# Kernel tuning notes

Measured on AMD Instinct MI355X. Metric: run time of the kernel, lower is better.

Reference implementation:

```python
import jax, jax.numpy as jnp
import numpy as np

EPS = 1e-8
LN_EPS = 1e-5
NEG = -1e9
H, E, D, P = 4, 32, 8, 64          # heads, embed_dim, head_dim, particles (= input_dim)
N_LAYERS, N_CLS = 4, 2
N_BATCH = 2048
F_EXTRA = 60                        # x feature channels; F_EXTRA + 4 == P == input_dim


def _ln(x):
    m = jnp.mean(x, -1, keepdims=True)
    v = jnp.mean((x - m) ** 2, -1, keepdims=True)
    return (x - m) * jax.lax.rsqrt(v + LN_EPS)


def _lin(x, w, b):
    return x @ w.T + b


def _gelu(x):
    return jax.nn.gelu(x, approximate=False)


def _mha(q_in, kv, in_w, in_b, out_w, out_b, attn_bias, kpm):
    # torch nn.MultiheadAttention, batch_first=False. q_in: (L,N,E), kv: (S,N,E)
    L, N, _ = q_in.shape
    S = kv.shape[0]
    q = _lin(q_in, in_w[:E], in_b[:E]) * (D ** -0.5)
    k = _lin(kv, in_w[E:2 * E], in_b[E:2 * E])
    v = _lin(kv, in_w[2 * E:], in_b[2 * E:])
    q = q.reshape(L, N, H, D); k = k.reshape(S, N, H, D); v = v.reshape(S, N, H, D)
    s = jnp.einsum('lnhd,snhd->nhls', q, k)
    if attn_bias is not None:
        s = s + attn_bias.reshape(N, H, L, S)
    s = jnp.where(kpm[:, None, None, :], NEG, s)
    a = jax.nn.softmax(s, -1)
    o = jnp.einsum('nhls,snhd->lnhd', a, v).reshape(L, N, E)
    return _lin(o, out_w, out_b)


def _jet_features(v):
    # vectorized calculate_jet_features_; v: (N,4,P). All pair features are symmetric,
    # diagonal stays zero (python loop skipped i==j), features are detached.
    e, px, py, pz = v[:, 0], v[:, 1], v[:, 2], v[:, 3]
    pt = jnp.sqrt(px ** 2 + py ** 2 + EPS)
    y = 0.5 * jnp.log((e + pz + EPS) / (e - pz + EPS))
    phi = jnp.mod(jnp.arctan2(py, px + EPS), 2.0 * np.pi)   # already in [0, 2pi)
    r = lambda a: a[:, :, None]
    c = lambda a: a[:, None, :]
    dist = (r(px) + c(px)) ** 2 + (r(py) + c(py)) ** 2 + (r(pz) + c(pz)) ** 2
    delta = jnp.sqrt(jnp.abs((r(y) - c(y)) ** 2 + (r(phi) - c(phi)) ** 2))
    pmin = jnp.minimum(r(pt), c(pt))
    kt = pmin * delta
    z = pmin / (r(pt) + c(pt) + EPS)
    m2 = r(e) ** 2 + c(e) ** 2 - dist
    f = jnp.stack([delta, kt, z, m2], axis=1)               # (N,4,P,P)
    f = f * (1.0 - jnp.eye(v.shape[2], dtype=f.dtype))
    return jax.lax.stop_gradient(f)


def _conv2d(x, w, b, stride, pad):
    y = jax.lax.conv_general_dilated(x, w, (stride, stride), [(pad, pad), (pad, pad)],
                                     dimension_numbers=('NCHW', 'OIHW', 'NCHW'))
    return y + b[None, :, None, None]


def _forward(x, four_momenta, jet_inputs, bn_w, bn_b, e1_w, e1_b, e2_w, e2_b,
             c1_w, c1_b, c2_w, c2_b,
             pb_in_w, pb_in_b, pb_out_w, pb_out_b, pb_f1_w, pb_f1_b, pb_f2_w, pb_f2_b, pb_wres,
             cb_in_w, cb_in_b, cb_out_w, cb_out_b, cb_f1_w, cb_f1_b, cb_f2_w, cb_f2_b, cb_wres,
             cb_cattn, cls_token, norm_w, norm_b, m1_w, m1_b, mh_w, mh_b, mf_w, mf_b):
    N = x.shape[0]
    xc = jnp.concatenate([x, four_momenta], axis=1)                 # (N, P, P): channels == particles
    kpm = ~(jnp.arange(P)[None, :] < jet_inputs[:, 1][:, None])     # (N, P) True = padded key
    xb = jnp.transpose(xc, (0, 2, 1))                               # (N, C=P, L=input_dim)
    mu = jnp.mean(xb, axis=(0, 2), keepdims=True)
    var = jnp.var(xb, axis=(0, 2), keepdims=True)
    xb = (xb - mu) * jax.lax.rsqrt(var + LN_EPS) * bn_w[None, :, None] + bn_b[None, :, None]
    h = jnp.transpose(xb, (2, 0, 1))                                # (seq, N, P)
    h = _gelu(_lin(_ln(h), e1_w, e1_b))
    h = _gelu(_lin(_ln(h), e2_w, e2_b))                             # (P, N, E)
    # --- PairEmbed: pairwise kinematic features -> 2 convs -> per-head attention bias
    f = _jet_features(four_momenta)                                 # (N, 4, P, P)
    cpe = _conv2d(f, c1_w, c1_b, 4, 0)                              # (N, H, 16, 16)
    cpe = _conv2d(cpe, c2_w, c2_b, 2, 1)                            # (N, H, 9, 9)
    bias = cpe.reshape(N * H, 9, 9)
    bias = jnp.pad(bias, ((0, 0), (0, P - 9), (0, P - 9)))          # additive bias zero-padded to (N*H,P,P)
    # --- particle blocks
    for i in range(N_LAYERS):
        res = h
        a = _ln(h)
        a = _mha(a, a, pb_in_w[i], pb_in_b[i], pb_out_w[i], pb_out_b[i], bias, kpm)
        h = _ln(a) + res
        res = h
        g = _gelu(_lin(_ln(h), pb_f1_w[i], pb_f1_b[i]))
        g = _lin(_ln(g), pb_f2_w[i], pb_f2_b[i])
        h = g + pb_wres[i] * res
    # --- class-attention blocks
    kpm_cls = jnp.concatenate([jnp.zeros((N, 1), dtype=bool), kpm], axis=1)
    cls = jnp.broadcast_to(cls_token, (1, N, E))
    for i in range(N_CLS):
        res = cls
        u = _ln(jnp.concatenate([cls, h], axis=0))                  # pre_attn_norm on keys/values only
        a = _mha(cls, u, cb_in_w[i], cb_in_b[i], cb_out_w[i], cb_out_b[i], None, kpm_cls)
        # tbhd,h->tbdh then reshape flattens as (d, h) order, matching torch
        a = jnp.einsum('tbhd,h->tbdh', a.reshape(1, N, H, D), cb_cattn[i]).reshape(1, N, E)
        cls = _ln(a) + res
        res = cls
        g = _gelu(_lin(_ln(cls), cb_f1_w[i], cb_f1_b[i]))
        g = _lin(_ln(g), cb_f2_w[i], cb_f2_b[i])
        cls = g + cb_wres[i] * res
    # --- head: affine LayerNorm + MLP (the two transposes in MLP cancel)
    z = (_ln(cls) * norm_w + norm_b)[0]                             # (N, E)
    z = jax.nn.relu(_lin(z, m1_w, m1_b))
    z = jax.nn.relu(_lin(z, mh_w, mh_b))
    z = jax.nn.sigmoid(_lin(z, mf_w, mf_b))                         # (N, 1)
    return z.reshape(-1)


def setup_inputs():
    key = jax.random.key(0)
    ks = jax.random.split(key, 40)
    w = lambda k, s: (0.05 * jax.random.normal(k, s)).astype(jnp.float32)
    p3 = jax.random.normal(ks[0], (N_BATCH, 3, P), dtype=jnp.float32)
    en = jnp.sqrt(jnp.sum(p3 ** 2, axis=1, keepdims=True) + 0.1)    # physical: E > |pz|
    four_momenta = jnp.concatenate([en, p3], axis=1)
    return {
        'x': jax.random.normal(ks[1], (N_BATCH, F_EXTRA, P), dtype=jnp.float32),
        'four_momenta': four_momenta,
        'jet_inputs': jax.random.randint(ks[2], (N_BATCH, 2), 1, P + 1),
        'bn_w': jnp.ones((P,), jnp.float32), 'bn_b': jnp.zeros((P,), jnp.float32),
        'e1_w': w(ks[3], (64, P)), 'e1_b': w(ks[4], (64,)),
        'e2_w': w(ks[5], (E, 64)), 'e2_b': w(ks[6], (E,)),
        'c1_w': w(ks[7], (H, 4, 4, 4)), 'c1_b': w(ks[8], (H,)),
        'c2_w': w(ks[9], (H, H, 2, 2)), 'c2_b': w(ks[10], (H,)),
        'pb_in_w': w(ks[11], (N_LAYERS, 3 * E, E)), 'pb_in_b': w(ks[12], (N_LAYERS, 3 * E)),
        'pb_out_w': w(ks[13], (N_LAYERS, E, E)), 'pb_out_b': w(ks[14], (N_LAYERS, E)),
        'pb_f1_w': w(ks[15], (N_LAYERS, 2 * E, E)), 'pb_f1_b': w(ks[16], (N_LAYERS, 2 * E)),
        'pb_f2_w': w(ks[17], (N_LAYERS, E, 2 * E)), 'pb_f2_b': w(ks[18], (N_LAYERS, E)),
        'pb_wres': jnp.ones((N_LAYERS, E), jnp.float32),
        'cb_in_w': w(ks[19], (N_CLS, 3 * E, E)), 'cb_in_b': w(ks[20], (N_CLS, 3 * E)),
        'cb_out_w': w(ks[21], (N_CLS, E, E)), 'cb_out_b': w(ks[22], (N_CLS, E)),
        'cb_f1_w': w(ks[23], (N_CLS, 2 * E, E)), 'cb_f1_b': w(ks[24], (N_CLS, 2 * E)),
        'cb_f2_w': w(ks[25], (N_CLS, E, 2 * E)), 'cb_f2_b': w(ks[26], (N_CLS, E)),
        'cb_wres': jnp.ones((N_CLS, E), jnp.float32),
        'cb_cattn': jnp.ones((N_CLS, H), jnp.float32),
        'cls_token': w(ks[27], (1, 1, E)),
        'norm_w': jnp.ones((E,), jnp.float32), 'norm_b': jnp.zeros((E,), jnp.float32),
        'm1_w': w(ks[28], (32, E)), 'm1_b': w(ks[29], (32,)),
        'mh_w': w(ks[30], (32, 32)), 'mh_b': w(ks[31], (32,)),
        'mf_w': w(ks[32], (1, 32)), 'mf_b': w(ks[33], (1,)),
    }


def reference(x, four_momenta, jet_inputs, bn_w, bn_b, e1_w, e1_b, e2_w, e2_b,
              c1_w, c1_b, c2_w, c2_b,
              pb_in_w, pb_in_b, pb_out_w, pb_out_b, pb_f1_w, pb_f1_b, pb_f2_w, pb_f2_b, pb_wres,
              cb_in_w, cb_in_b, cb_out_w, cb_out_b, cb_f1_w, cb_f1_b, cb_f2_w, cb_f2_b, cb_wres,
              cb_cattn, cls_token, norm_w, norm_b, m1_w, m1_b, mh_w, mh_b, mf_w, mf_b):
    return _forward(x, four_momenta, jet_inputs, bn_w, bn_b, e1_w, e1_b, e2_w, e2_b,
                    c1_w, c1_b, c2_w, c2_b,
                    pb_in_w, pb_in_b, pb_out_w, pb_out_b, pb_f1_w, pb_f1_b, pb_f2_w, pb_f2_b, pb_wres,
                    cb_in_w, cb_in_b, cb_out_w, cb_out_b, cb_f1_w, cb_f1_b, cb_f2_w, cb_f2_b, cb_wres,
                    cb_cattn, cls_token, norm_w, norm_b, m1_w, m1_b, mh_w, mh_b, mf_w, mf_b)
```

## Files before the change

### kernel.cpp

```cpp
#include <hip/hip_runtime.h>


__device__ __forceinline__ float4 ld4(const float* p){ return *reinterpret_cast<const float4*>(p); }
__device__ __forceinline__ void st4(float* p, float4 v){ *reinterpret_cast<float4*>(p) = v; }
__device__ __forceinline__ float dot4(float4 a, float4 b){ return a.x*b.x + a.y*b.y + a.z*b.z + a.w*b.w; }
__device__ __forceinline__ float geluf(float v){ return 0.5f*v*(1.0f + erff(v*0.70710678118654752f)); }

__global__ void bn_stats_partial(const float* __restrict__ x, const float* __restrict__ fm,
                                 float* __restrict__ part) {
  int p  = threadIdx.x & 63;
  int rg = threadIdx.x >> 6;
  float s = 0.f, s2 = 0.f;
  for (int R = blockIdx.x*4 + rg; R < 2048*64; R += 1024) {
    int n_ = R >> 6, c = R & 63;
    float v = (c < 60) ? x[n_*3840 + c*64 + p] : fm[n_*256 + (c-60)*64 + p];
    s += v; s2 += v*v;
  }
  __shared__ float sm[256], sm2[256];
  sm[threadIdx.x] = s; sm2[threadIdx.x] = s2;
  __syncthreads();
  if (threadIdx.x < 64) {
    part[blockIdx.x*128 + p]      = sm[p]+sm[64+p]+sm[128+p]+sm[192+p];
    part[blockIdx.x*128 + 64 + p] = sm2[p]+sm2[64+p]+sm2[128+p]+sm2[192+p];
  }
// ... 148 lines not shown
        }
      }
    }
    G_bias[n*324 + idx] = s;
  }
  {
    int p4 = (tid & 15) * 4;
    float sc0 = SSTAT[p4], sc1 = SSTAT[p4+1], sc2 = SSTAT[p4+2], sc3 = SSTAT[p4+3];
    float sh0 = SSTAT[64+p4], sh1 = SSTAT[64+p4+1], sh2 = SSTAT[64+p4+2], sh3 = SSTAT[64+p4+3];
    for (int c = tid>>4; c < 64; c += 16) {
      float4 v = (c < 60) ? ld4(x + n*3840 + c*64 + p4) : ld4(fm + n*256 + (c-60)*64 + p4);
      st4(&SX[c*68 + p4], make_float4(v.x*sc0+sh0, v.y*sc1+sh1, v.z*sc2+sh2, v.w*sc3+sh3));
    }
  }
  __syncthreads();

  if (wact) ln_rows64(SX, SY, tid);
  for (int idx = tid; idx < 1024; idx += 256) st4(&SW[(idx>>4)*68 + (idx&15)*4], ld4(e1w + idx*4));
  if (tid < 64) SW[4352+tid] = e1b[tid];
  __syncthreads();

  {
    int tg = tid>>4, og = tid&15;
    float acc[4][4];
    #pragma unroll
    for (int o=0;o<4;o++){ float b = SW[4352+o*16+og];
      #pragma unroll
      for (int i=0;i<4;i++) acc[i][o] = b; }
    if (wact) {
      #pragma unroll 2
      for (int j=0;j<64;j+=4){
        float4 av[4], wv[4];
        #pragma unroll
        for (int i=0;i<4;i++) av[i] = ld4(SY + (tg*4+i)*68 + j);
        #pragma unroll
        for (int o=0;o<4;o++) wv[o] = ld4(SW + (o*16+og)*68 + j);
        #pragma unroll
        for (int i=0;i<4;i++)
          #pragma unroll
          for (int o=0;o<4;o++) acc[i][o] += dot4(av[i], wv[o]);
      }
    }
    __syncthreads();
    if (wact) {
      #pragma unroll
      for (int i=0;i<4;i++)
        #pragma unroll
        for (int o=0;o<4;o++) SX[(tg*4+i)*68 + o*16+og] = geluf(acc[i][o]);
    }
  }
  __syncthreads();

  if (wact) ln_rows64(SX, SY, tid);
  for (int idx = tid; idx < 512; idx += 256) st4(&SW[(idx>>4)*68 + (idx&15)*4], ld4(e2w + idx*4));
  if (tid < 32) SW[4352+tid] = e2b[tid];
  __syncthreads();

  if (wact) {
    int tg = tid>>4, og = tid&15;
    float acc[4][2];
    #pragma unroll
    for (int o=0;o<2;o++){ float b = SW[4352+o*16+og];
      #pragma unroll
      for (int i=0;i<4;i++) acc[i][o] = b; }
    #pragma unroll 2
    for (int j=0;j<64;j+=4){
      float4 av[4], wv[2];
      #pragma unroll
      for (int i=0;i<4;i++) av[i] = ld4(SY + (tg*4+i)*68 + j);
      #pragma unroll
      for (int o=0;o<2;o++) wv[o] = ld4(SW + (o*16+og)*68 + j);
      #pragma unroll
      for (int i=0;i<4;i++)
        #pragma unroll
        for (int o=0;o<2;o++) acc[i][o] += dot4(av[i], wv[o]);
    }
    #pragma unroll
    for (int i=0;i<4;i++)
      #pragma unroll
      for (int o=0;o<2;o++) G_h[n*2048 + (tg*4+i)*32 + o*16+og] = geluf(acc[i][o]);
  }
}

__global__ __launch_bounds__(256, 4) void k_layer(
    const int* __restrict__ ji,
    const float* __restrict__ in_w,  const float* __restrict__ in_b,
    const float* __restrict__ out_w, const float* __restrict__ out_b,
    const float* __restrict__ f1w,   const float* __restrict__ f1b,
    const float* __restrict__ f2w,   const float* __restrict__ f2b,
    const float* __restrict__ wres,
    float* __restrict__ G_h, const float* __restrict__ G_bias)
{
  const int n   = blockIdx.x;
  const int tid = threadIdx.x;
  const int njet = ji[n*2+1];
  const bool wact = ((tid>>6)<<4) < njet;
  const int r_ = tid>>2, g_ = tid&3;

  __shared__ __align__(16) float SX[64*36];
  __shared__ __align__(16) float SY[64*68];
  __shared__ __align__(16) float SW[3584];

  float b9[9];
  {
    int hh = tid>>6, l = tid&63;
    if (l < 9) {
      #pragma unroll
      for (int j=0;j<9;j++) b9[j] = G_bias[n*324 + hh*81 + l*9 + j];
    } else {
      #pragma unroll
      for (int j=0;j<9;j++) b9[j] = 0.f;
    }
  }
  float4 h0 = make_float4(0,0,0,0), h1 = make_float4(0,0,0,0);
  if (wact) {
    h0 = ld4(G_h + n*2048 + r_*32 + g_*8);
    h1 = ld4(G_h + n*2048 + r_*32 + g_*8 + 4);
  }

  if (wact) {
    float s = h0.x+h0.y+h0.z+h0.w + h1.x+h1.y+h1.z+h1.w;
    s += __shfl_xor(s,1); s += __shfl_xor(s,2);
    float mean = s * 0.03125f;
    float4 da = make_float4(h0.x-mean,h0.y-mean,h0.z-mean,h0.w-mean);
    float4 db = make_float4(h1.x-mean,h1.y-mean,h1.z-mean,h1.w-mean);
    float q = dot4(da,da) + dot4(db,db);
    q += __shfl_xor(q,1); q += __shfl_xor(q,2);
    float irs = rsqrtf(q*0.03125f + 1e-5f);
    st4(&SX[r_*36 + g_*8],   make_float4(da.x*irs, da.y*irs, da.z*irs, da.w*irs));
    st4(&SX[r_*36 + g_*8+4], make_float4(db.x*irs, db.y*irs, db.z*irs, db.w*irs));
  }
  for (int idx = tid; idx < 768; idx += 256) st4(&SW[(idx>>3)*36 + (idx&7)*4], ld4(in_w + idx*4));
  if (tid < 96) SW[3456+tid] = in_b[tid];
  __syncthreads();

  if (wact) {
    int tg = tid>>4, og = tid&15;
    float acc[4][4];
    #pragma unroll
    for (int o=0;o<4;o++){ float b = SW[3456+32+o*16+og];
      #pragma unroll
      for (int i=0;i<4;i++) acc[i][o] = b; }
    #pragma unroll 2
    for (int j=0;j<32;j+=4){
      float4 av[4], wv[4];
      #pragma unroll
      for (int i=0;i<4;i++) av[i] = ld4(SX + (tg*4+i)*36 + j);
      #pragma unroll
      for (int o=0;o<4;o++) wv[o] = ld4(SW + (32+o*16+og)*36 + j);
      #pragma unroll
      for (int i=0;i<4;i++)
        #pragma unroll
        for (int o=0;o<4;o++) acc[i][o] += dot4(av[i], wv[o]);
    }
    #pragma unroll
    for (int i=0;i<4;i++)
      #pragma unroll
      for (int o=0;o<4;o++){
        int ew = 32 + o*16+og, t = tg*4+i;
        if (ew < 64) SY[(ew-32)*68 + t] = acc[i][o];
        else         SY[2176 + (ew-64)*68 + t] = acc[i][o];
      }
  }
  __syncthreads();

  float od[8];
  {
    int hh = tid>>6, l = tid&63;
    float qd[8];
    #pragma unroll
    for (int d=0;d<8;d++){
      int e = hh*8+d;
      float a_ = SW[3456+e];
      #pragma unroll
      for (int k=0;k<8;k++) a_ += dot4(ld4(SX + l*36 + k*4), ld4(SW + e*36 + k*4));
      qd[d] = a_ * 0.35355339059327373f;
    }
    float m = -3.4e38f, lsum = 0.f;
    #pragma unroll
    for (int d=0;d<8;d++) od[d] = 0.f;
    #pragma unroll 1
    for (int s0 = 0; s0 < njet; s0 += 16) {
      float sc[16];
      #pragma unroll
      for (int j=0;j<16;j++) sc[j]=0.f;
      #pragma unroll
      for (int d=0;d<8;d++){
        const float* kr = SY + (hh*8+d)*68 + s0;
        float qv = qd[d];
        #pragma unroll
        for (int j=0;j<16;j+=4){
          float4 kv4 = ld4(kr+j);
          sc[j]  +=qv*kv4.x; sc[j+1]+=qv*kv4.y;
          sc[j+2]+=qv*kv4.z; sc[j+3]+=qv*kv4.w;
        }
      }
      float cm = -3.4e38f;
      if (s0 != 0 && s0 + 16 <= njet) {
        #pragma unroll
        for (int j=0;j<16;j++) cm = fmaxf(cm, sc[j]);
      } else {
        #pragma unroll
        for (int j=0;j<16;j++){
          int s = s0+j;
          float a_ = sc[j];
          if (s0 == 0 && l < 9 && j < 9) a_ += b9[j];
          a_ = (s >= njet) ? -1000000000.0f : a_;
          sc[j] = a_;
          cm = fmaxf(cm, a_);
        }
      }
      float nm = fmaxf(m, cm);
      float corr = __expf(m - nm);
      lsum *= corr;
      #pragma unroll
      for (int d=0;d<8;d++) od[d] *= corr;
      #pragma unroll
      for (int j=0;j<16;j++){ sc[j] = __expf(sc[j]-nm); lsum += sc[j]; }
      #pragma unroll
      for (int d=0;d<8;d++){
        const float* vr = SY + 2176 + (hh*8+d)*68 + s0;
        float a_ = 0.f;
        #pragma unroll
        for (int j=0;j<16;j+=4){
          float4 vv = ld4(vr+j);
          a_ += sc[j]*vv.x + sc[j+1]*vv.y + sc[j+2]*vv.z + sc[j+3]*vv.w;
        }
        od[d] += a_;
      }
      m = nm;
    }
    float inv = 1.f/lsum;
    #pragma unroll
    for (int d=0;d<8;d++) od[d] *= inv;
  }
  __syncthreads();
  {
    int hh = tid>>6, l = tid&63;
    st4(&SX[l*36 + hh*8],     make_float4(od[0],od[1],od[2],od[3]));
    st4(&SX[l*36 + hh*8 + 4], make_float4(od[4],od[5],od[6],od[7]));
  }
  for (int idx = tid; idx < 256; idx += 256) st4(&SW[(idx>>3)*36 + (idx&7)*4], ld4(out_w + idx*4));
  if (tid < 32) SW[3456+tid] = out_b[tid];
  __syncthreads();

  if (wact) {
    int tg = tid>>4, og = tid&15;
    float acc[4][2];
    #pragma unroll
    for (int o=0;o<2;o++){ float b = SW[3456+o*16+og];
      #pragma unroll
      for (int i=0;i<4;i++) acc[i][o] = b; }
    #pragma unroll 2
    for (int j=0;j<32;j+=4){
      float4 av[4], wv[2];
      #pragma unroll
      for (int i=0;i<4;i++) av[i] = ld4(SX + (tg*4+i)*36 + j);
      #pragma unroll
      for (int o=0;o<2;o++) wv[o] = ld4(SW + (o*16+og)*36 + j);
      #pragma unroll
      for (int i=0;i<4;i++)
        #pragma unroll
        for (int o=0;o<2;o++) acc[i][o] += dot4(av[i], wv[o]);
    }
    #pragma unroll
    for (int i=0;i<4;i++)
      #pragma unroll
      for (int o=0;o<2;o++) SY[(tg*4+i)*36 + o*16+og] = acc[i][o];
  }
  __syncthreads();

  if (wact) {
    const float* row = SY + r_*36 + g_*8;
    float4 a = ld4(row), b = ld4(row+4);
    float s = a.x+a.y+a.z+a.w + b.x+b.y+b.z+b.w;
    s += __shfl_xor(s,1); s += __shfl_xor(s,2);
    float mean = s * 0.03125f;
    float4 da = make_float4(a.x-mean,a.y-mean,a.z-mean,a.w-mean);
    float4 db = make_float4(b.x-mean,b.y-mean,b.z-mean,b.w-mean);
    float q = dot4(da,da) + dot4(db,db);
    q += __shfl_xor(q,1); q += __shfl_xor(q,2);
    float irs = rsqrtf(q*0.03125f + 1e-5f);
    h0 = make_float4(da.x*irs+h0.x, da.y*irs+h0.y, da.z*irs+h0.z, da.w*irs+h0.w);
    h1 = make_float4(db.x*irs+h1.x, db.y*irs+h1.y, db.z*irs+h1.z, db.w*irs+h1.w);
    float s2 = h0.x+h0.y+h0.z+h0.w + h1.x+h1.y+h1.z+h1.w;
    s2 += __shfl_xor(s2,1); s2 += __shfl_xor(s2,2);
    float mean2 = s2 * 0.03125f;
    float4 ea = make_float4(h0.x-mean2,h0.y-mean2,h0.z-mean2,h0.w-mean2);
    float4 eb = make_float4(h1.x-mean2,h1.y-mean2,h1.z-mean2,h1.w-mean2);
    float q2 = dot4(ea,ea) + dot4(eb,eb);
    q2 += __shfl_xor(q2,1); q2 += __shfl_xor(q2,2);
    float irs2 = rsqrtf(q2*0.03125f + 1e-5f);
    st4(&SX[r_*36 + g_*8],   make_float4(ea.x*irs2, ea.y*irs2, ea.z*irs2, ea.w*irs2));
    st4(&SX[r_*36 + g_*8+4], make_float4(eb.x*irs2, eb.y*irs2, eb.z*irs2, eb.w*irs2));
  }
  for (int idx = tid; idx < 512; idx += 256) st4(&SW[(idx>>3)*36 + (idx&7)*4], ld4(f1w + idx*4));
  if (tid < 64) SW[3456+tid] = f1b[tid];
  __syncthreads();

  if (wact) {
    int tg = tid>>4, og = tid&15;
    float acc[4][4];
    #pragma unroll
    for (int o=0;o<4;o++){ float b = SW[3456+o*16+og];
      #pragma unroll
      for (int i=0;i<4;i++) acc[i][o] = b; }
    #pragma unroll 2
    for (int j=0;j<32;j+=4){
      float4 av[4], wv[4];
      #pragma unroll
      for (int i=0;i<4;i++) av[i] = ld4(SX + (tg*4+i)*36 + j);
      #pragma unroll
      for (int o=0;o<4;o++) wv[o] = ld4(SW + (o*16+og)*36 + j);
      #pragma unroll
      for (int i=0;i<4;i++)
        #pragma unroll
        for (int o=0;o<4;o++) acc[i][o] += dot4(av[i], wv[o]);
    }
    #pragma unroll
    for (int i=0;i<4;i++)
      #pragma unroll
      for (int o=0;o<4;o++) SY[(tg*4+i)*68 + o*16+og] = geluf(acc[i][o]);
  }
  __syncthreads();

  if (wact) {
    float* row = SY + r_*68 + g_*16;
    float4 v0 = ld4(row), v1 = ld4(row+4), v2 = ld4(row+8), v3 = ld4(row+12);
    float s = v0.x+v0.y+v0.z+v0.w + v1.x+v1.y+v1.z+v1.w
            + v2.x+v2.y+v2.z+v2.w + v3.x+v3.y+v3.z+v3.w;
    s += __shfl_xor(s,1); s += __shfl_xor(s,2);
    float mean = s * 0.015625f;
    float4 d0 = make_float4(v0.x-mean,v0.y-mean,v0.z-mean,v0.w-mean);
    float4 d1 = make_float4(v1.x-mean,v1.y-mean,v1.z-mean,v1.w-mean);
    float4 d2 = make_float4(v2.x-mean,v2.y-mean,v2.z-mean,v2.w-mean);
    float4 d3 = make_float4(v3.x-mean,v3.y-mean,v3.z-mean,v3.w-mean);
    float q = dot4(d0,d0)+dot4(d1,d1)+dot4(d2,d2)+dot4(d3,d3);
    q += __shfl_xor(q,1); q += __shfl_xor(q,2);
    float irs = rsqrtf(q*0.015625f + 1e-5f);
    st4(row,    make_float4(d0.x*irs,d0.y*irs,d0.z*irs,d0.w*irs));
    st4(row+4,  make_float4(d1.x*irs,d1.y*irs,d1.z*irs,d1.w*irs));
    st4(row+8,  make_float4(d2.x*irs,d2.y*irs,d2.z*irs,d2.w*irs));
    st4(row+12, make_float4(d3.x*irs,d3.y*irs,d3.z*irs,d3.w*irs));
  }
  for (int idx = tid; idx < 512; idx += 256) st4(&SW[(idx>>4)*68 + (idx&15)*4], ld4(f2w + idx*4));
  if (tid < 32){ SW[3456+tid] = f2b[tid]; SW[3488+tid] = wres[tid]; }
  __syncthreads();

  if (wact) {
    int tg = tid>>4, og = tid&15;
    float acc[4][2];
    #pragma unroll
    for (int o=0;o<2;o++){ float b = SW[3456+o*16+og];
      #pragma unroll
      for (int i=0;i<4;i++) acc[i][o] = b; }
    #pragma unroll 2
    for (int j=0;j<64;j+=4){
      float4 av[4], wv[2];
      #pragma unroll
      for (int i=0;i<4;i++) av[i] = ld4(SY + (tg*4+i)*68 + j);
      #pragma unroll
      for (int o=0;o<2;o++) wv[o] = ld4(SW + (o*16+og)*68 + j);
      #pragma unroll
      for (int i=0;i<4;i++)
        #pragma unroll
        for (int o=0;o<2;o++) acc[i][o] += dot4(av[i], wv[o]);
    }
    #pragma unroll
    for (int i=0;i<4;i++)
      #pragma unroll
      for (int o=0;o<2;o++) SX[(tg*4+i)*36 + o*16+og] = acc[i][o];
  }
  __syncthreads();

  if (wact) {
    float4 a0 = ld4(&SX[r_*36 + g_*8]),  a1 = ld4(&SX[r_*36 + g_*8 + 4]);
    float4 w0 = ld4(&SW[3488 + g_*8]),   w1 = ld4(&SW[3488 + g_*8 + 4]);
    st4(G_h + n*2048 + r_*32 + g_*8,
        make_float4(a0.x + w0.x*h0.x, a0.y + w0.y*h0.y, a0.z + w0.z*h0.z, a0.w + w0.w*h0.w));
    st4(G_h + n*2048 + r_*32 + g_*8 + 4,
        make_float4(a1.x + w1.x*h1.x, a1.y + w1.y*h1.y, a1.z + w1.z*h1.z, a1.w + w1.w*h1.w));
  }
}

__global__ __launch_bounds__(256, 3) void k_cls(
    const int* __restrict__ ji,
    const float* __restrict__ cb_in_w, const float* __restrict__ cb_in_b,
    const float* __restrict__ cb_out_w, const float* __restrict__ cb_out_b,
    const float* __restrict__ cb_f1_w, const float* __restrict__ cb_f1_b,
    const float* __restrict__ cb_f2_w, const float* __restrict__ cb_f2_b,
    const float* __restrict__ cb_wres, const float* __restrict__ cb_cattn,
    const float* __restrict__ cls_tok, const float* __restrict__ norm_w, const float* __restrict__ norm_b,
    const float* __restrict__ m1w, const float* __restrict__ m1b,
    const float* __restrict__ mhw, const float* __restrict__ mhb,
    const float* __restrict__ mfw, const float* __restrict__ mfb,
    const float* __restrict__ G_h, float* __restrict__ out)
{
  const int n   = blockIdx.x;
  const int tid = threadIdx.x;
  const int njet = ji[n*2+1];
  const int nt16 = (njet + 15) & ~15;
  const bool wact = ((tid>>6)<<4) < njet;

  __shared__ __align__(16) float SX[64*36];
  __shared__ __align__(16) float SY[64*68];
  __shared__ __align__(16) float SW[3584];
  __shared__ __align__(16) float SV[320];
  __shared__ __align__(16) float csh[32];

  for (int idx = tid; idx < (nt16<<3); idx += 256) {
    float4 v = ld4(G_h + n*2048 + idx*4);
    int t = idx>>3, e = (idx&7)*4;
    st4(&SX[t*36 + e], v);
  }
  __syncthreads();

  if (wact) ln_rows32(SX, SX, tid);
  if (tid < 32) csh[tid] = cls_tok[tid];
  __syncthreads();

  #pragma unroll 1
  for (int cl = 0; cl < 2; cl++) {
    const float* iw = cb_in_w + cl*3072;
    const float* ib = cb_in_b + cl*96;

    if (tid < 32) {
      float v = csh[tid];
      float s = v;
      s += __shfl_xor(s,1); s += __shfl_xor(s,2); s += __shfl_xor(s,4); s += __shfl_xor(s,8); s += __shfl_xor(s,16);
      float mean = s * 0.03125f;
      float d = v - mean;
      float q = d*d;
      q += __shfl_xor(q,1); q += __shfl_xor(q,2); q += __shfl_xor(q,4); q += __shfl_xor(q,8); q += __shfl_xor(q,16);
      float irs = rsqrtf(q*0.03125f + 1e-5f);
      SV[tid] = d*irs;
    }
    for (int idx = tid; idx < 768; idx += 256) st4(&SW[(idx>>3)*36 + (idx&7)*4], ld4(iw + idx*4));
    if (tid < 96) SW[3456+tid] = ib[tid];
    __syncthreads();

    if (tid < 32) {
      int e = tid;
      float a_ = SW[3456+e];
      #pragma unroll
      for (int k=0;k<8;k++) a_ += dot4(ld4(&csh[k*4]), ld4(SW + e*36 + k*4));
      SV[32+e] = a_ * 0.35355339059327373f;
    }
    if (tid < 64) {
      int ew = 32 + tid;
      float a_ = SW[3456+ew];
      #pragma unroll
      for (int k=0;k<8;k++) a_ += dot4(ld4(SV + k*4), ld4(SW + ew*36 + k*4));
      if (ew < 64) SY[(ew-32)*68] = a_;
      else         SY[2176 + (ew-64)*68] = a_;
    }
    {
      int tg = tid>>4, og = tid&15;
      if (wact) {
        float acc[4][4];
        #pragma unroll
        for (int o=0;o<4;o++){ float b = SW[3456+32+o*16+og];
          #pragma unroll
          for (int i=0;i<4;i++) acc[i][o] = b; }
        #pragma unroll 2
// ... 136 lines not shown
    float d = v - mean;
    float q = d*d;
    q += __shfl_xor(q,1); q += __shfl_xor(q,2); q += __shfl_xor(q,4); q += __shfl_xor(q,8); q += __shfl_xor(q,16);
    float irs = rsqrtf(q*0.03125f + 1e-5f);
    SV[tid] = d*irs*norm_w[tid] + norm_b[tid];
  }
  if (tid < 32) {
    float a_ = m1b[tid];
    const float* wrow = m1w + tid*32;
    #pragma unroll
    for (int j=0;j<32;j++) a_ += SV[j]*wrow[j];
    SV[64+tid] = fmaxf(a_, 0.f);
  }
  if (tid < 32) {
    float a_ = mhb[tid];
    const float* wrow = mhw + tid*32;
    #pragma unroll
    for (int j=0;j<32;j++) a_ += SV[64+j]*wrow[j];
    SV[128+tid] = fmaxf(a_, 0.f);
  }
  if (tid == 0) {
    float a_ = mfb[0];
    #pragma unroll
    for (int j=0;j<32;j++) a_ += SV[128+j]*mfw[j];
    out[n] = 1.f/(1.f + expf(-a_));
  }
}

extern "C" void kernel_launch(void* const* d_in, const int* in_sizes, int n_in,
                              void* d_out, int out_size, void* d_ws, size_t ws_size,
                              hipStream_t stream) {
  (void)in_sizes; (void)n_in; (void)out_size; (void)ws_size;
  const float* x     = (const float*)d_in[0];
  const float* fm    = (const float*)d_in[1];
  const int*   ji    = (const int*)  d_in[2];
  const float* bn_w  = (const float*)d_in[3];
  const float* bn_b  = (const float*)d_in[4];
  const float* e1w   = (const float*)d_in[5];
  const float* e1b   = (const float*)d_in[6];
  const float* e2w   = (const float*)d_in[7];
  const float* e2b   = (const float*)d_in[8];
  const float* c1w   = (const float*)d_in[9];
  const float* c1b   = (const float*)d_in[10];
  const float* c2w   = (const float*)d_in[11];
  const float* c2b   = (const float*)d_in[12];
  const float* pb_in_w  = (const float*)d_in[13];
  const float* pb_in_b  = (const float*)d_in[14];
  const float* pb_out_w = (const float*)d_in[15];
  const float* pb_out_b = (const float*)d_in[16];
  const float* pb_f1_w  = (const float*)d_in[17];
  const float* pb_f1_b  = (const float*)d_in[18];
  const float* pb_f2_w  = (const float*)d_in[19];
  const float* pb_f2_b  = (const float*)d_in[20];
  const float* pb_wres  = (const float*)d_in[21];
  const float* cb_in_w  = (const float*)d_in[22];
  const float* cb_in_b  = (const float*)d_in[23];
  const float* cb_out_w = (const float*)d_in[24];
  const float* cb_out_b = (const float*)d_in[25];
  const float* cb_f1_w  = (const float*)d_in[26];
  const float* cb_f1_b  = (const float*)d_in[27];
  const float* cb_f2_w  = (const float*)d_in[28];
  const float* cb_f2_b  = (const float*)d_in[29];
  const float* cb_wres  = (const float*)d_in[30];
  const float* cb_cattn = (const float*)d_in[31];
  const float* cls_tok  = (const float*)d_in[32];
  const float* norm_w   = (const float*)d_in[33];
  const float* norm_b   = (const float*)d_in[34];
  const float* m1w      = (const float*)d_in[35];
  const float* m1b      = (const float*)d_in[36];
  const float* mhw      = (const float*)d_in[37];
  const float* mhb      = (const float*)d_in[38];
  const float* mfw      = (const float*)d_in[39];
  const float* mfb      = (const float*)d_in[40];

  float* part   = (float*)d_ws;
  float* stats  = part + 32768;
  float* G_h    = part + 40960;
  float* G_bias = G_h + 2048*2048;

  bn_stats_partial<<<256, 256, 0, stream>>>(x, fm, part);
  bn_stats_final<<<1, 64, 0, stream>>>(part, stats);
  k_embed<<<2048, 256, 0, stream>>>(x, fm, ji, stats, bn_w, bn_b, e1w, e1b, e2w, e2b,
                                    c1w, c1b, c2w, c2b, G_h, G_bias);
  for (int li = 0; li < 4; li++) {
    k_layer<<<2048, 256, 0, stream>>>(ji,
        pb_in_w + li*3072, pb_in_b + li*96,
        pb_out_w + li*1024, pb_out_b + li*32,
        pb_f1_w + li*2048, pb_f1_b + li*64,
        pb_f2_w + li*2048, pb_f2_b + li*32,
        pb_wres + li*32, G_h, G_bias);
  }
  k_cls<<<2048, 256, 0, stream>>>(ji, cb_in_w, cb_in_b, cb_out_w, cb_out_b,
                                  cb_f1_w, cb_f1_b, cb_f2_w, cb_f2_b,
                                  cb_wres, cb_cattn, cls_tok, norm_w, norm_b,
                                  m1w, m1b, mhw, mhb, mfw, mfb, G_h, (float*)d_out);
}
```

Baseline: 480.0 us.

## Fuse four particle-attention layer launches into one persistent per-jet kernel

Merges the four per-layer k_layer launches into a single k_layers kernel that loops over layers inside each block. The hidden state h0/h1 stays in registers between layers, and the attention bias is loaded once. This removes three kernel launches and the global-memory round trip of the per-jet hidden state between layers. It adds a trailing barrier per layer iteration and makes the loop body longer, which could raise register pressure under the existing launch bounds.

```diff
diff --git a/kernel.cpp b/kernel.cpp
--- a/kernel.cpp
+++ b/kernel.cpp
@@ -254,13 +254,13 @@
   }
 }
 
-__global__ __launch_bounds__(256, 4) void k_layer(
+__global__ __launch_bounds__(256, 4) void k_layers(
     const int* __restrict__ ji,
-    const float* __restrict__ in_w,  const float* __restrict__ in_b,
-    const float* __restrict__ out_w, const float* __restrict__ out_b,
-    const float* __restrict__ f1w,   const float* __restrict__ f1b,
-    const float* __restrict__ f2w,   const float* __restrict__ f2b,
-    const float* __restrict__ wres,
+    const float* __restrict__ pb_in_w,  const float* __restrict__ pb_in_b,
+    const float* __restrict__ pb_out_w, const float* __restrict__ pb_out_b,
+    const float* __restrict__ pb_f1_w,  const float* __restrict__ pb_f1_b,
+    const float* __restrict__ pb_f2_w,  const float* __restrict__ pb_f2_b,
+    const float* __restrict__ pb_wres,
     float* __restrict__ G_h, const float* __restrict__ G_bias)
 {
   const int n   = blockIdx.x;
@@ -290,268 +290,285 @@
     h1 = ld4(G_h + n*2048 + r_*32 + g_*8 + 4);
   }
 
+  #pragma unroll 1
+  for (int li = 0; li < 4; li++) {
+    const float* in_w  = pb_in_w  + li*3072;
+    const float* in_b  = pb_in_b  + li*96;
+    const float* out_w = pb_out_w + li*1024;
+    const float* out_b = pb_out_b + li*32;
+    const float* f1w   = pb_f1_w  + li*2048;
+    const float* f1b   = pb_f1_b  + li*64;
+    const float* f2w   = pb_f2_w  + li*2048;
+    const float* f2b   = pb_f2_b  + li*32;
+    const float* wres  = pb_wres  + li*32;
+
+    if (wact) {
+      float s = h0.x+h0.y+h0.z+h0.w + h1.x+h1.y+h1.z+h1.w;
+      s += __shfl_xor(s,1); s += __shfl_xor(s,2);
+      float mean = s * 0.03125f;
+      float4 da = make_float4(h0.x-mean,h0.y-mean,h0.z-mean,h0.w-mean);
+      float4 db = make_float4(h1.x-mean,h1.y-mean,h1.z-mean,h1.w-mean);
+      float q = dot4(da,da) + dot4(db,db);
+      q += __shfl_xor(q,1); q += __shfl_xor(q,2);
+      float irs = rsqrtf(q*0.03125f + 1e-5f);
+      st4(&SX[r_*36 + g_*8],   make_float4(da.x*irs, da.y*irs, da.z*irs, da.w*irs));
+      st4(&SX[r_*36 + g_*8+4], make_float4(db.x*irs, db.y*irs, db.z*irs, db.w*irs));
+    }
+    for (int idx = tid; idx < 768; idx += 256) st4(&SW[(idx>>3)*36 + (idx&7)*4], ld4(in_w + idx*4));
+    if (tid < 96) SW[3456+tid] = in_b[tid];
+    __syncthreads();
+
+    if (wact) {
+      int tg = tid>>4, og = tid&15;
+      float acc[4][4];
+      #pragma unroll
+      for (int o=0;o<4;o++){ float b = SW[3456+32+o*16+og];
+        #pragma unroll
+        for (int i=0;i<4;i++) acc[i][o] = b; }
+      #pragma unroll 2
+      for (int j=0;j<32;j+=4){
+        float4 av[4], wv[4];
+        #pragma unroll
+        for (int i=0;i<4;i++) av[i] = ld4(SX + (tg*4+i)*36 + j);
+        #pragma unroll
+        for (int o=0;o<4;o++) wv[o] = ld4(SW + (32+o*16+og)*36 + j);
+        #pragma unroll
+        for (int i=0;i<4;i++)
+          #pragma unroll
+          for (int o=0;o<4;o++) acc[i][o] += dot4(av[i], wv[o]);
+      }
+      #pragma unroll
+      for (int i=0;i<4;i++)
+        #pragma unroll
+        for (int o=0;o<4;o++){
+          int ew = 32 + o*16+og, t = tg*4+i;
+          if (ew < 64) SY[(ew-32)*68 + t] = acc[i][o];
+          else         SY[2176 + (ew-64)*68 + t] = acc[i][o];
+        }
+    }
+    __syncthreads();
+
+    float od[8];
+    {
+      int hh = tid>>6, l = tid&63;
+      float qd[8];
+      #pragma unroll
+      for (int d=0;d<8;d++){
+        int e = hh*8+d;
+        float a_ = SW[3456+e];
+        #pragma unroll
+        for (int k=0;k<8;k++) a_ += dot4(ld4(SX + l*36 + k*4), ld4(SW + e*36 + k*4));
+        qd[d] = a_ * 0.35355339059327373f;
+      }
+      float m = -3.4e38f, lsum = 0.f;
+      #pragma unroll
+      for (int d=0;d<8;d++) od[d] = 0.f;
+      #pragma unroll 1
+      for (int s0 = 0; s0 < njet; s0 += 16) {
+        float sc[16];
+        #pragma unroll
+        for (int j=0;j<16;j++) sc[j]=0.f;
+        #pragma unroll
+        for (int d=0;d<8;d++){
+          const float* kr = SY + (hh*8+d)*68 + s0;
+          float qv = qd[d];
+          #pragma unroll
+          for (int j=0;j<16;j+=4){
+            float4 kv4 = ld4(kr+j);
+            sc[j]  +=qv*kv4.x; sc[j+1]+=qv*kv4.y;
+            sc[j+2]+=qv*kv4.z; sc[j+3]+=qv*kv4.w;
+          }
+        }
+        float cm = -3.4e38f;
+        if (s0 != 0 && s0 + 16 <= njet) {
+          #pragma unroll
+          for (int j=0;j<16;j++) cm = fmaxf(cm, sc[j]);
+        } else {
+          #pragma unroll
+          for (int j=0;j<16;j++){
+            int s = s0+j;
+            float a_ = sc[j];
+            if (s0 == 0 && l < 9 && j < 9) a_ += b9[j];
+            a_ = (s >= njet) ? -1000000000.0f : a_;
+            sc[j] = a_;
+            cm = fmaxf(cm, a_);
+          }
+        }
+        float nm = fmaxf(m, cm);
+        float corr = __expf(m - nm);
+        lsum *= corr;
+        #pragma unroll
+        for (int d=0;d<8;d++) od[d] *= corr;
+        #pragma unroll
+        for (int j=0;j<16;j++){ sc[j] = __expf(sc[j]-nm); lsum += sc[j]; }
+        #pragma unroll
+        for (int d=0;d<8;d++){
+          const float* vr = SY + 2176 + (hh*8+d)*68 + s0;
+          float a_ = 0.f;
+          #pragma unroll
+          for (int j=0;j<16;j+=4){
+            float4 vv = ld4(vr+j);
+            a_ += sc[j]*vv.x + sc[j+1]*vv.y + sc[j+2]*vv.z + sc[j+3]*vv.w;
+          }
+          od[d] += a_;
+        }
+        m = nm;
+      }
+      float inv = 1.f/lsum;
+      #pragma unroll
+      for (int d=0;d<8;d++) od[d] *= inv;
+    }
+    __syncthreads();
+    {
+      int hh = tid>>6, l = tid&63;
+      st4(&SX[l*36 + hh*8],     make_float4(od[0],od[1],od[2],od[3]));
+      st4(&SX[l*36 + hh*8 + 4], make_float4(od[4],od[5],od[6],od[7]));
+    }
+    for (int idx = tid; idx < 256; idx += 256) st4(&SW[(idx>>3)*36 + (idx&7)*4], ld4(out_w + idx*4));
+    if (tid < 32) SW[3456+tid] = out_b[tid];
+    __syncthreads();
+
+    if (wact) {
+      int tg = tid>>4, og = tid&15;
+      float acc[4][2];
+      #pragma unroll
+      for (int o=0;o<2;o++){ float b = SW[3456+o*16+og];
+        #pragma unroll
+        for (int i=0;i<4;i++) acc[i][o] = b; }
+      #pragma unroll 2
+      for (int j=0;j<32;j+=4){
+        float4 av[4], wv[2];
+        #pragma unroll
+        for (int i=0;i<4;i++) av[i] = ld4(SX + (tg*4+i)*36 + j);
+        #pragma unroll
+        for (int o=0;o<2;o++) wv[o] = ld4(SW + (o*16+og)*36 + j);
+        #pragma unroll
+        for (int i=0;i<4;i++)
+          #pragma unroll
+          for (int o=0;o<2;o++) acc[i][o] += dot4(av[i], wv[o]);
+      }
+      #pragma unroll
+      for (int i=0;i<4;i++)
+        #pragma unroll
+        for (int o=0;o<2;o++) SY[(tg*4+i)*36 + o*16+og] = acc[i][o];
+    }
+    __syncthreads();
+
+    if (wact) {
+      const float* row = SY + r_*36 + g_*8;
+      float4 a = ld4(row), b = ld4(row+4);
+      float s = a.x+a.y+a.z+a.w + b.x+b.y+b.z+b.w;
+      s += __shfl_xor(s,1); s += __shfl_xor(s,2);
+      float mean = s * 0.03125f;
+      float4 da = make_float4(a.x-mean,a.y-mean,a.z-mean,a.w-mean);
+      float4 db = make_float4(b.x-mean,b.y-mean,b.z-mean,b.w-mean);
+      float q = dot4(da,da) + dot4(db,db);
+      q += __shfl_xor(q,1); q += __shfl_xor(q,2);
+      float irs = rsqrtf(q*0.03125f + 1e-5f);
+      h0 = make_float4(da.x*irs+h0.x, da.y*irs+h0.y, da.z*irs+h0.z, da.w*irs+h0.w);
+      h1 = make_float4(db.x*irs+h1.x, db.y*irs+h1.y, db.z*irs+h1.z, db.w*irs+h1.w);
+      float s2 = h0.x+h0.y+h0.z+h0.w + h1.x+h1.y+h1.z+h1.w;
+      s2 += __shfl_xor(s2,1); s2 += __shfl_xor(s2,2);
+      float mean2 = s2 * 0.03125f;
+      float4 ea = make_float4(h0.x-mean2,h0.y-mean2,h0.z-mean2,h0.w-mean2);
+      float4 eb = make_float4(h1.x-mean2,h1.y-mean2,h1.z-mean2,h1.w-mean2);
+      float q2 = dot4(ea,ea) + dot4(eb,eb);
+      q2 += __shfl_xor(q2,1); q2 += __shfl_xor(q2,2);
+      float irs2 = rsqrtf(q2*0.03125f + 1e-5f);
+      st4(&SX[r_*36 + g_*8],   make_float4(ea.x*irs2, ea.y*irs2, ea.z*irs2, ea.w*irs2));
+      st4(&SX[r_*36 + g_*8+4], make_float4(eb.x*irs2, eb.y*irs2, eb.z*irs2, eb.w*irs2));
+    }
+    for (int idx = tid; idx < 512; idx += 256) st4(&SW[(idx>>3)*36 + (idx&7)*4], ld4(f1w + idx*4));
+    if (tid < 64) SW[3456+tid] = f1b[tid];
+    __syncthreads();
+
+    if (wact) {
+      int tg = tid>>4, og = tid&15;
+      float acc[4][4];
+      #pragma unroll
+      for (int o=0;o<4;o++){ float b = SW[3456+o*16+og];
+        #pragma unroll
+        for (int i=0;i<4;i++) acc[i][o] = b; }
+      #pragma unroll 2
+      for (int j=0;j<32;j+=4){
+        float4 av[4], wv[4];
+        #pragma unroll
+        for (int i=0;i<4;i++) av[i] = ld4(SX + (tg*4+i)*36 + j);
+        #pragma unroll
+        for (int o=0;o<4;o++) wv[o] = ld4(SW + (o*16+og)*36 + j);
+        #pragma unroll
+        for (int i=0;i<4;i++)
+          #pragma unroll
+          for (int o=0;o<4;o++) acc[i][o] += dot4(av[i], wv[o]);
+      }
+      #pragma unroll
+      for (int i=0;i<4;i++)
+        #pragma unroll
+        for (int o=0;o<4;o++) SY[(tg*4+i)*68 + o*16+og] = geluf(acc[i][o]);
+    }
+    __syncthreads();
+
+    if (wact) {
+      float* row = SY + r_*68 + g_*16;
+      float4 v0 = ld4(row), v1 = ld4(row+4), v2 = ld4(row+8), v3 = ld4(row+12);
+      float s = v0.x+v0.y+v0.z+v0.w + v1.x+v1.y+v1.z+v1.w
+              + v2.x+v2.y+v2.z+v2.w + v3.x+v3.y+v3.z+v3.w;
+      s += __shfl_xor(s,1); s += __shfl_xor(s,2);
+      float mean = s * 0.015625f;
+      float4 d0 = make_float4(v0.x-mean,v0.y-mean,v0.z-mean,v0.w-mean);
+      float4 d1 = make_float4(v1.x-mean,v1.y-mean,v1.z-mean,v1.w-mean);
+      float4 d2 = make_float4(v2.x-mean,v2.y-mean,v2.z-mean,v2.w-mean);
+      float4 d3 = make_float4(v3.x-mean,v3.y-mean,v3.z-mean,v3.w-mean);
+      float q = dot4(d0,d0)+dot4(d1,d1)+dot4(d2,d2)+dot4(d3,d3);
+      q += __shfl_xor(q,1); q += __shfl_xor(q,2);
+      float irs = rsqrtf(q*0.015625f + 1e-5f);
+      st4(row,    make_float4(d0.x*irs,d0.y*irs,d0.z*irs,d0.w*irs));
+      st4(row+4,  make_float4(d1.x*irs,d1.y*irs,d1.z*irs,d1.w*irs));
+      st4(row+8,  make_float4(d2.x*irs,d2.y*irs,d2.z*irs,d2.w*irs));
+      st4(row+12, make_float4(d3.x*irs,d3.y*irs,d3.z*irs,d3.w*irs));
+    }
+    for (int idx = tid; idx < 512; idx += 256) st4(&SW[(idx>>4)*68 + (idx&15)*4], ld4(f2w + idx*4));
+    if (tid < 32){ SW[3456+tid] = f2b[tid]; SW[3488+tid] = wres[tid]; }
+    __syncthreads();
+
+    if (wact) {
+      int tg = tid>>4, og = tid&15;
+      float acc[4][2];
+      #pragma unroll
+      for (int o=0;o<2;o++){ float b = SW[3456+o*16+og];
+        #pragma unroll
+        for (int i=0;i<4;i++) acc[i][o] = b; }
+      #pragma unroll 2
+      for (int j=0;j<64;j+=4){
+        float4 av[4], wv[2];
+        #pragma unroll
+        for (int i=0;i<4;i++) av[i] = ld4(SY + (tg*4+i)*68 + j);
+        #pragma unroll
+        for (int o=0;o<2;o++) wv[o] = ld4(SW + (o*16+og)*68 + j);
+        #pragma unroll
+        for (int i=0;i<4;i++)
+          #pragma unroll
+          for (int o=0;o<2;o++) acc[i][o] += dot4(av[i], wv[o]);
+      }
+      #pragma unroll
+      for (int i=0;i<4;i++)
+        #pragma unroll
+        for (int o=0;o<2;o++) SX[(tg*4+i)*36 + o*16+og] = acc[i][o];
+    }
+    __syncthreads();
+
+    if (wact) {
+      float4 a0 = ld4(&SX[r_*36 + g_*8]),  a1 = ld4(&SX[r_*36 + g_*8 + 4]);
+      float4 w0 = ld4(&SW[3488 + g_*8]),   w1 = ld4(&SW[3488 + g_*8 + 4]);
+      h0 = make_float4(a0.x + w0.x*h0.x, a0.y + w0.y*h0.y, a0.z + w0.z*h0.z, a0.w + w0.w*h0.w);
+      h1 = make_float4(a1.x + w1.x*h1.x, a1.y + w1.y*h1.y, a1.z + w1.z*h1.z, a1.w + w1.w*h1.w);
+    }
+    __syncthreads();
+  }
+
   if (wact) {
-    float s = h0.x+h0.y+h0.z+h0.w + h1.x+h1.y+h1.z+h1.w;
-    s += __shfl_xor(s,1); s += __shfl_xor(s,2);
-    float mean = s * 0.03125f;
-    float4 da = make_float4(h0.x-mean,h0.y-mean,h0.z-mean,h0.w-mean);
-    float4 db = make_float4(h1.x-mean,h1.y-mean,h1.z-mean,h1.w-mean);
-    float q = dot4(da,da) + dot4(db,db);
-    q += __shfl_xor(q,1); q += __shfl_xor(q,2);
-    float irs = rsqrtf(q*0.03125f + 1e-5f);
-    st4(&SX[r_*36 + g_*8],   make_float4(da.x*irs, da.y*irs, da.z*irs, da.w*irs));
-    st4(&SX[r_*36 + g_*8+4], make_float4(db.x*irs, db.y*irs, db.z*irs, db.w*irs));
-  }
-  for (int idx = tid; idx < 768; idx += 256) st4(&SW[(idx>>3)*36 + (idx&7)*4], ld4(in_w + idx*4));
-  if (tid < 96) SW[3456+tid] = in_b[tid];
-  __syncthreads();
-
-  if (wact) {
-    int tg = tid>>4, og = tid&15;
-    float acc[4][4];
-    #pragma unroll
-    for (int o=0;o<4;o++){ float b = SW[3456+32+o*16+og];
-      #pragma unroll
-      for (int i=0;i<4;i++) acc[i][o] = b; }
-    #pragma unroll 2
-    for (int j=0;j<32;j+=4){
-      float4 av[4], wv[4];
-      #pragma unroll
-      for (int i=0;i<4;i++) av[i] = ld4(SX + (tg*4+i)*36 + j);
-      #pragma unroll
-      for (int o=0;o<4;o++) wv[o] = ld4(SW + (32+o*16+og)*36 + j);
-      #pragma unroll
-      for (int i=0;i<4;i++)
-        #pragma unroll
-        for (int o=0;o<4;o++) acc[i][o] += dot4(av[i], wv[o]);
-    }
-    #pragma unroll
-    for (int i=0;i<4;i++)
-      #pragma unroll
-      for (int o=0;o<4;o++){
-        int ew = 32 + o*16+og, t = tg*4+i;
-        if (ew < 64) SY[(ew-32)*68 + t] = acc[i][o];
-        else         SY[2176 + (ew-64)*68 + t] = acc[i][o];
-      }
-  }
-  __syncthreads();
-
-  float od[8];
-  {
-    int hh = tid>>6, l = tid&63;
-    float qd[8];
-    #pragma unroll
-    for (int d=0;d<8;d++){
-      int e = hh*8+d;
-      float a_ = SW[3456+e];
-      #pragma unroll
-      for (int k=0;k<8;k++) a_ += dot4(ld4(SX + l*36 + k*4), ld4(SW + e*36 + k*4));
-      qd[d] = a_ * 0.35355339059327373f;
-    }
-    float m = -3.4e38f, lsum = 0.f;
-    #pragma unroll
-    for (int d=0;d<8;d++) od[d] = 0.f;
-    #pragma unroll 1
-    for (int s0 = 0; s0 < njet; s0 += 16) {
-      float sc[16];
-      #pragma unroll
-      for (int j=0;j<16;j++) sc[j]=0.f;
-      #pragma unroll
-      for (int d=0;d<8;d++){
-        const float* kr = SY + (hh*8+d)*68 + s0;
-        float qv = qd[d];
-        #pragma unroll
-        for (int j=0;j<16;j+=4){
-          float4 kv4 = ld4(kr+j);
-          sc[j]  +=qv*kv4.x; sc[j+1]+=qv*kv4.y;
-          sc[j+2]+=qv*kv4.z; sc[j+3]+=qv*kv4.w;
-        }
-      }
-      float cm = -3.4e38f;
-      if (s0 != 0 && s0 + 16 <= njet) {
-        #pragma unroll
-        for (int j=0;j<16;j++) cm = fmaxf(cm, sc[j]);
-      } else {
-        #pragma unroll
-        for (int j=0;j<16;j++){
-          int s = s0+j;
-          float a_ = sc[j];
-          if (s0 == 0 && l < 9 && j < 9) a_ += b9[j];
-          a_ = (s >= njet) ? -1000000000.0f : a_;
-          sc[j] = a_;
-          cm = fmaxf(cm, a_);
-        }
-      }
-      float nm = fmaxf(m, cm);
-      float corr = __expf(m - nm);
-      lsum *= corr;
-      #pragma unroll
-      for (int d=0;d<8;d++) od[d] *= corr;
-      #pragma unroll
-      for (int j=0;j<16;j++){ sc[j] = __expf(sc[j]-nm); lsum += sc[j]; }
-      #pragma unroll
-      for (int d=0;d<8;d++){
-        const float* vr = SY + 2176 + (hh*8+d)*68 + s0;
-        float a_ = 0.f;
-        #pragma unroll
-        for (int j=0;j<16;j+=4){
-          float4 vv = ld4(vr+j);
-          a_ += sc[j]*vv.x + sc[j+1]*vv.y + sc[j+2]*vv.z + sc[j+3]*vv.w;
-        }
-        od[d] += a_;
-      }
-      m = nm;
-    }
-    float inv = 1.f/lsum;
-    #pragma unroll
-    for (int d=0;d<8;d++) od[d] *= inv;
-  }
-  __syncthreads();
-  {
-    int hh = tid>>6, l = tid&63;
-    st4(&SX[l*36 + hh*8],     make_float4(od[0],od[1],od[2],od[3]));
-    st4(&SX[l*36 + hh*8 + 4], make_float4(od[4],od[5],od[6],od[7]));
-  }
-  for (int idx = tid; idx < 256; idx += 256) st4(&SW[(idx>>3)*36 + (idx&7)*4], ld4(out_w + idx*4));
-  if (tid < 32) SW[3456+tid] = out_b[tid];
-  __syncthreads();
-
-  if (wact) {
-    int tg = tid>>4, og = tid&15;
-    float acc[4][2];
-    #pragma unroll
-    for (int o=0;o<2;o++){ float b = SW[3456+o*16+og];
-      #pragma unroll
-      for (int i=0;i<4;i++) acc[i][o] = b; }
-    #pragma unroll 2
-    for (int j=0;j<32;j+=4){
-      float4 av[4], wv[2];
-      #pragma unroll
-      for (int i=0;i<4;i++) av[i] = ld4(SX + (tg*4+i)*36 + j);
-      #pragma unroll
-      for (int o=0;o<2;o++) wv[o] = ld4(SW + (o*16+og)*36 + j);
-      #pragma unroll
-      for (int i=0;i<4;i++)
-        #pragma unroll
-        for (int o=0;o<2;o++) acc[i][o] += dot4(av[i], wv[o]);
-    }
-    #pragma unroll
-    for (int i=0;i<4;i++)
-      #pragma unroll
-      for (int o=0;o<2;o++) SY[(tg*4+i)*36 + o*16+og] = acc[i][o];
-  }
-  __syncthreads();
-
-  if (wact) {
-    const float* row = SY + r_*36 + g_*8;
-    float4 a = ld4(row), b = ld4(row+4);
-    float s = a.x+a.y+a.z+a.w + b.x+b.y+b.z+b.w;
-    s += __shfl_xor(s,1); s += __shfl_xor(s,2);
-    float mean = s * 0.03125f;
-    float4 da = make_float4(a.x-mean,a.y-mean,a.z-mean,a.w-mean);
-    float4 db = make_float4(b.x-mean,b.y-mean,b.z-mean,b.w-mean);
-    float q = dot4(da,da) + dot4(db,db);
-    q += __shfl_xor(q,1); q += __shfl_xor(q,2);
-    float irs = rsqrtf(q*0.03125f + 1e-5f);
-    h0 = make_float4(da.x*irs+h0.x, da.y*irs+h0.y, da.z*irs+h0.z, da.w*irs+h0.w);
-    h1 = make_float4(db.x*irs+h1.x, db.y*irs+h1.y, db.z*irs+h1.z, db.w*irs+h1.w);
-    float s2 = h0.x+h0.y+h0.z+h0.w + h1.x+h1.y+h1.z+h1.w;
-    s2 += __shfl_xor(s2,1); s2 += __shfl_xor(s2,2);
-    float mean2 = s2 * 0.03125f;
-    float4 ea = make_float4(h0.x-mean2,h0.y-mean2,h0.z-mean2,h0.w-mean2);
-    float4 eb = make_float4(h1.x-mean2,h1.y-mean2,h1.z-mean2,h1.w-mean2);
-    float q2 = dot4(ea,ea) + dot4(eb,eb);
-    q2 += __shfl_xor(q2,1); q2 += __shfl_xor(q2,2);
-    float irs2 = rsqrtf(q2*0.03125f + 1e-5f);
-    st4(&SX[r_*36 + g_*8],   make_float4(ea.x*irs2, ea.y*irs2, ea.z*irs2, ea.w*irs2));
-    st4(&SX[r_*36 + g_*8+4], make_float4(eb.x*irs2, eb.y*irs2, eb.z*irs2, eb.w*irs2));
-  }
-  for (int idx = tid; idx < 512; idx += 256) st4(&SW[(idx>>3)*36 + (idx&7)*4], ld4(f1w + idx*4));
-  if (tid < 64) SW[3456+tid] = f1b[tid];
-  __syncthreads();
-
-  if (wact) {
-    int tg = tid>>4, og = tid&15;
-    float acc[4][4];
-    #pragma unroll
-    for (int o=0;o<4;o++){ float b = SW[3456+o*16+og];
-      #pragma unroll
-      for (int i=0;i<4;i++) acc[i][o] = b; }
-    #pragma unroll 2
-    for (int j=0;j<32;j+=4){
-      float4 av[4], wv[4];
-      #pragma unroll
-      for (int i=0;i<4;i++) av[i] = ld4(SX + (tg*4+i)*36 + j);
-      #pragma unroll
-      for (int o=0;o<4;o++) wv[o] = ld4(SW + (o*16+og)*36 + j);
-      #pragma unroll
-      for (int i=0;i<4;i++)
-        #pragma unroll
-        for (int o=0;o<4;o++) acc[i][o] += dot4(av[i], wv[o]);
-    }
-    #pragma unroll
-    for (int i=0;i<4;i++)
-      #pragma unroll
-      for (int o=0;o<4;o++) SY[(tg*4+i)*68 + o*16+og] = geluf(acc[i][o]);
-  }
-  __syncthreads();
-
-  if (wact) {
-    float* row = SY + r_*68 + g_*16;
-    float4 v0 = ld4(row), v1 = ld4(row+4), v2 = ld4(row+8), v3 = ld4(row+12);
-    float s = v0.x+v0.y+v0.z+v0.w + v1.x+v1.y+v1.z+v1.w
-            + v2.x+v2.y+v2.z+v2.w + v3.x+v3.y+v3.z+v3.w;
-    s += __shfl_xor(s,1); s += __shfl_xor(s,2);
-    float mean = s * 0.015625f;
-    float4 d0 = make_float4(v0.x-mean,v0.y-mean,v0.z-mean,v0.w-mean);
-    float4 d1 = make_float4(v1.x-mean,v1.y-mean,v1.z-mean,v1.w-mean);
-    float4 d2 = make_float4(v2.x-mean,v2.y-mean,v2.z-mean,v2.w-mean);
-    float4 d3 = make_float4(v3.x-mean,v3.y-mean,v3.z-mean,v3.w-mean);
-    float q = dot4(d0,d0)+dot4(d1,d1)+dot4(d2,d2)+dot4(d3,d3);
-    q += __shfl_xor(q,1); q += __shfl_xor(q,2);
-    float irs = rsqrtf(q*0.015625f + 1e-5f);
-    st4(row,    make_float4(d0.x*irs,d0.y*irs,d0.z*irs,d0.w*irs));
-    st4(row+4,  make_float4(d1.x*irs,d1.y*irs,d1.z*irs,d1.w*irs));
-    st4(row+8,  make_float4(d2.x*irs,d2.y*irs,d2.z*irs,d2.w*irs));
-    st4(row+12, make_float4(d3.x*irs,d3.y*irs,d3.z*irs,d3.w*irs));
-  }
-  for (int idx = tid; idx < 512; idx += 256) st4(&SW[(idx>>4)*68 + (idx&15)*4], ld4(f2w + idx*4));
-  if (tid < 32){ SW[3456+tid] = f2b[tid]; SW[3488+tid] = wres[tid]; }
-  __syncthreads();
-
-  if (wact) {
-    int tg = tid>>4, og = tid&15;
-    float acc[4][2];
-    #pragma unroll
-    for (int o=0;o<2;o++){ float b = SW[3456+o*16+og];
-      #pragma unroll
-      for (int i=0;i<4;i++) acc[i][o] = b; }
-    #pragma unroll 2
-    for (int j=0;j<64;j+=4){
-      float4 av[4], wv[2];
-      #pragma unroll
-      for (int i=0;i<4;i++) av[i] = ld4(SY + (tg*4+i)*68 + j);
-      #pragma unroll
-      for (int o=0;o<2;o++) wv[o] = ld4(SW + (o*16+og)*68 + j);
-      #pragma unroll
-      for (int i=0;i<4;i++)
-        #pragma unroll
-        for (int o=0;o<2;o++) acc[i][o] += dot4(av[i], wv[o]);
-    }
-    #pragma unroll
-    for (int i=0;i<4;i++)
-      #pragma unroll
-      for (int o=0;o<2;o++) SX[(tg*4+i)*36 + o*16+og] = acc[i][o];
-  }
-  __syncthreads();
-
-  if (wact) {
-    float4 a0 = ld4(&SX[r_*36 + g_*8]),  a1 = ld4(&SX[r_*36 + g_*8 + 4]);
-    float4 w0 = ld4(&SW[3488 + g_*8]),   w1 = ld4(&SW[3488 + g_*8 + 4]);
-    st4(G_h + n*2048 + r_*32 + g_*8,
-        make_float4(a0.x + w0.x*h0.x, a0.y + w0.y*h0.y, a0.z + w0.z*h0.z, a0.w + w0.w*h0.w));
-    st4(G_h + n*2048 + r_*32 + g_*8 + 4,
-        make_float4(a1.x + w1.x*h1.x, a1.y + w1.y*h1.y, a1.z + w1.z*h1.z, a1.w + w1.w*h1.w));
+    st4(G_h + n*2048 + r_*32 + g_*8,     h0);
+    st4(G_h + n*2048 + r_*32 + g_*8 + 4, h1);
   }
 }
 
@@ -854,14 +871,9 @@
   bn_stats_final<<<1, 64, 0, stream>>>(part, stats);
   k_embed<<<2048, 256, 0, stream>>>(x, fm, ji, stats, bn_w, bn_b, e1w, e1b, e2w, e2b,
                                     c1w, c1b, c2w, c2b, G_h, G_bias);
-  for (int li = 0; li < 4; li++) {
-    k_layer<<<2048, 256, 0, stream>>>(ji,
-        pb_in_w + li*3072, pb_in_b + li*96,
-        pb_out_w + li*1024, pb_out_b + li*32,
-        pb_f1_w + li*2048, pb_f1_b + li*64,
-        pb_f2_w + li*2048, pb_f2_b + li*32,
-        pb_wres + li*32, G_h, G_bias);
-  }
+  k_layers<<<2048, 256, 0, stream>>>(ji,
+      pb_in_w, pb_in_b, pb_out_w, pb_out_b,
+      pb_f1_w, pb_f1_b, pb_f2_w, pb_f2_b, pb_wres, G_h, G_bias);
   k_cls<<<2048, 256, 0, stream>>>(ji, cb_in_w, cb_in_b, cb_out_w, cb_out_b,
                                   cb_f1_w, cb_f1_b, cb_f2_w, cb_f2_b,
                                   cb_wres, cb_cattn, cls_tok, norm_w, norm_b,
```

Result: slower. 535.0 us (+11.5%).
